# Kernel tuning notes

Hardware: AMD Instinct MI355X
Metric: run time of the kernel (lower is better)

## Reference

```python
import jax, jax.numpy as jnp
import numpy as np

SCALAR_DIM = 452          # 2 + 6 + (110+1)*4
GRID_C, GRID_H, GRID_W = 2, 32, 18
GRID_FLAT = GRID_C * GRID_H * GRID_W  # 1152
OBS_DIM = SCALAR_DIM + GRID_FLAT      # 1604
CNN_OUT, SC_OUT, HID, N_ACT = 128, 64, 128, 2305
CNN_FLAT = 64 * 8 * 5                 # 32x18 -> 16x9 -> 8x5
T, B = 256, 128


def setup_inputs() -> dict:
    key = jax.random.key(0)
    ks = jax.random.split(key, 24)
    p = lambda k, shape: jax.random.normal(k, shape, jnp.float32) * 0.02
    return dict(
        obs_seq=jax.random.uniform(ks[0], (T, B, OBS_DIM), jnp.float32),
        h0=jnp.zeros((1, B, HID), jnp.float32),
        c0=jnp.zeros((1, B, HID), jnp.float32),
        done_mask=jax.random.randint(ks[1], (T, B), 0, 2) > 0,
        conv1_w=p(ks[2], (32, GRID_C, 3, 3)), conv1_b=jnp.zeros((32,), jnp.float32),
        conv2_w=p(ks[3], (64, 32, 3, 3)),     conv2_b=jnp.zeros((64,), jnp.float32),
        conv3_w=p(ks[4], (64, 64, 3, 3)),     conv3_b=jnp.zeros((64,), jnp.float32),
        fc_w=p(ks[5], (CNN_OUT, CNN_FLAT)),   fc_b=jnp.zeros((CNN_OUT,), jnp.float32),
        s1_w=p(ks[6], (64, SCALAR_DIM)),      s1_b=jnp.zeros((64,), jnp.float32),
        s2_w=p(ks[7], (SC_OUT, 64)),          s2_b=jnp.zeros((SC_OUT,), jnp.float32),
        w_ih=p(ks[8], (4 * HID, CNN_OUT + SC_OUT)),
        w_hh=p(ks[9], (4 * HID, HID)),
        b_ih=jnp.zeros((4 * HID,), jnp.float32),
        b_hh=jnp.zeros((4 * HID,), jnp.float32),
        pol_w=p(ks[10], (N_ACT, HID)), pol_b=jnp.zeros((N_ACT,), jnp.float32),
        val_w=p(ks[11], (1, HID)),     val_b=jnp.zeros((1,), jnp.float32),
    )


def _conv(x, w, b, stride):
    y = jax.lax.conv_general_dilated(
        x, w, (stride, stride), ((1, 1), (1, 1)),
        dimension_numbers=("NCHW", "OIHW", "NCHW"))
    return y + b[None, :, None, None]


def reference(obs_seq, h0, c0, done_mask,
              conv1_w, conv1_b, conv2_w, conv2_b, conv3_w, conv3_b,
              fc_w, fc_b, s1_w, s1_b, s2_w, s2_b,
              w_ih, w_hh, b_ih, b_hh, pol_w, pol_b, val_w, val_b):
    Tt, Bb, _ = obs_seq.shape
    flat = obs_seq.reshape(Tt * Bb, -1)
    scalars = flat[:, :SCALAR_DIM]
    grid = flat[:, SCALAR_DIM:SCALAR_DIM + GRID_FLAT].reshape(-1, GRID_C, GRID_H, GRID_W)

    # CNN encoder
    x = jax.nn.relu(_conv(grid, conv1_w, conv1_b, 1))
    x = jax.nn.relu(_conv(x, conv2_w, conv2_b, 2))
    x = jax.nn.relu(_conv(x, conv3_w, conv3_b, 2))
    cnn = jax.nn.relu(x.reshape(x.shape[0], -1) @ fc_w.T + fc_b)

    # scalar MLP
    sc = jax.nn.relu(jax.nn.relu(scalars @ s1_w.T + s1_b) @ s2_w.T + s2_b)

    emb = jnp.concatenate([cnn, sc], axis=-1).reshape(Tt, Bb, -1)  # (T,B,192)

    # episode-reset mask applied BEFORE each step (for t>0, from done[t-1])
    keep = jnp.concatenate(
        [jnp.ones((1, Bb), jnp.float32),
         1.0 - done_mask[:-1].astype(jnp.float32)], axis=0)[..., None]  # (T,B,1)

    def step(carry, inp):
        h, c = carry
        x_t, k_t = inp
        h = h * k_t
        c = c * k_t
        g = x_t @ w_ih.T + h @ w_hh.T + b_ih + b_hh
        i, f, gg, o = jnp.split(g, 4, axis=-1)  # torch gate order i,f,g,o
        c = jax.nn.sigmoid(f) * c + jax.nn.sigmoid(i) * jnp.tanh(gg)
        h = jax.nn.sigmoid(o) * jnp.tanh(c)
        return (h, c), h

    (h_f, c_f), outs = jax.lax.scan(step, (h0[0], c0[0]), (emb, keep))

    logits = outs @ pol_w.T + pol_b   # (T,B,n_actions)
    values = outs @ val_w.T + val_b   # (T,B,1)
    return logits, values, h_f[None], c_f[None]
```

## Files before the change

kernel.cpp:

```cpp
#include <hip/hip_runtime.h>


typedef __attribute__((ext_vector_type(8))) short v8s;
typedef __attribute__((ext_vector_type(4))) float v4f;
typedef __attribute__((ext_vector_type(4))) unsigned int v4u;

#define DEV static __device__ __forceinline__

DEV unsigned int cvtpk(float lo, float hi){
  unsigned int d;
  asm("v_cvt_pk_bf16_f32 %0, %1, %2" : "=v"(d) : "v"(lo), "v"(hi));
  return d;
}
DEV unsigned short f2bf(float x){ return (unsigned short)(cvtpk(x, x) & 0xffffu); }
DEV float bf2f(unsigned short h){ return __uint_as_float(((unsigned int)h) << 16); }
DEV unsigned int pkbf(float a, float b){ return cvtpk(a, b); }
DEV v4f MFMA(v8s a, v8s b, v4f c){ return __builtin_amdgcn_mfma_f32_16x16x32_bf16(a, b, c, 0, 0, 0); }
DEV v4f vzero(){ v4f z = {0.f, 0.f, 0.f, 0.f}; return z; }
DEV float relu(float x){ return x > 0.f ? x : 0.f; }
DEV float sigm(float x){ return 1.0f / (1.0f + __expf(-x)); }
DEV float tanhfast(float x){
  x = fminf(15.0f, fmaxf(-15.0f, x));
  float e = __expf(2.0f * x);
  return (e - 1.0f) / (e + 1.0f);
}
DEV uint2 pack4(v4f a, float4 b){
  return make_uint2(cvtpk(relu(a[0]+b.x), relu(a[1]+b.y)),
                    cvtpk(relu(a[2]+b.z), relu(a[3]+b.w)));
}
union U8S { v4u u4; v8s s8; };

__global__ __launch_bounds__(256) void pack_all(
    const float* __restrict__ c1w, const float* __restrict__ c2w,
    const float* __restrict__ c3w, const float* __restrict__ fcw,
    const float* __restrict__ s1w, const float* __restrict__ s2w,
    const float* __restrict__ wih, const float* __restrict__ whh,
    const float* __restrict__ pw,
    unsigned short* __restrict__ w1p, unsigned short* __restrict__ w2p,
    unsigned short* __restrict__ w3p, unsigned short* __restrict__ fcp,
    unsigned short* __restrict__ s1p, unsigned short* __restrict__ s2p,
    unsigned short* __restrict__ lsp, unsigned short* __restrict__ pop){
  int b = blockIdx.x;
  const float *src, *src2 = nullptr; unsigned short* dst;
  int N, K, KS, CI, mode, rel;
  if      (b < 4)   { src=c1w; dst=w1p; N=32;  K=24;  KS=1;  CI=2;  mode=4; rel=b; }
  else if (b < 76)  { src=c2w; dst=w2p; N=64;  K=288; KS=9;  CI=32; mode=1; rel=b-4; }
  else if (b < 220) { src=c3w; dst=w3p; N=64;  K=576; KS=18; CI=64; mode=1; rel=b-76; }
  else if (b < 1500){ src=fcw; dst=fcp; N=128; K=2560;KS=80; CI=0;  mode=2; rel=b-220; }
  else if (b < 1620){ src=s1w; dst=s1p; N=64;  K=452; KS=15; CI=0;  mode=0; rel=b-1500; }
  else if (b < 1636){ src=s2w; dst=s2p; N=64;  K=64;  KS=2;  CI=0;  mode=0; rel=b-1620; }
  else if (b < 2276){ src=wih; src2=whh; dst=lsp; N=512; K=320; KS=10; CI=0; mode=3; rel=b-1636; }
  else              { src=pw;  dst=pop; N=2305;K=128; KS=4;  CI=0;  mode=0; rel=b-2276; }
  int idx = rel * 256 + threadIdx.x;
  int e  = idx & 7;
  int l  = (idx >> 3) & 63;
  int fs = idx >> 9;
  int ks = fs % KS;
  int nt = fs / KS;
  int n = nt * 16 + (l & 15);
  int k = ks * 32 + (l >> 4) * 8 + e;
  float v = 0.f;
  if (n < N && k < K){
    if (mode == 0)      v = src[n * K + k];
    else if (mode == 1){ int p9 = k / CI, ci = k - p9 * CI; v = src[(n * CI + ci) * 9 + p9]; }
    else if (mode == 2){ int pos = k >> 6, ci = k & 63;     v = src[n * 2560 + ci * 40 + pos]; }
    else if (mode == 3) v = (k < 192) ? src[n * 192 + k] : src2[n * 128 + (k - 192)];
    else { int dy = k >> 3, r = k & 7, dx = r >> 1, ci = r & 1;
           if (dx < 3) v = src[(n * 2 + ci) * 9 + dy * 3 + dx]; }
  }
  dst[idx] = f2bf(v);
}

__global__ __launch_bounds__(512) void bias_kernel(const float* __restrict__ bih,
    const float* __restrict__ bhh, float* __restrict__ bias512){
  int t = threadIdx.x;
  if (t < 512) bias512[t] = bih[t] + bhh[t];
}

__global__ __launch_bounds__(256) void mlp_kernel(const float* __restrict__ obs,
    const unsigned short* __restrict__ s1p, const unsigned short* __restrict__ s2p,
    const float* __restrict__ s1b, const float* __restrict__ s2b,
    unsigned short* __restrict__ emb){
  __shared__ __align__(16) unsigned short xl[32 * 488];
  __shared__ __align__(16) unsigned short h1[32 * 72];
  int tid = threadIdx.x, w = tid >> 6, l = tid & 63, i = l & 15, u = l >> 4;
  long s0 = (long)blockIdx.x * 32;
  for (int idx = tid; idx < 32 * 113; idx += 256){
    int r = idx / 113, q = idx - r * 113;
    float4 v = *(const float4*)&obs[(s0 + r) * 1604 + q * 4];
    *(uint2*)&xl[r * 488 + q * 4] = make_uint2(pkbf(v.x, v.y), pkbf(v.z, v.w));
  }
  for (int idx = tid; idx < 32 * 28; idx += 256){
    int r = idx / 28, k = 452 + (idx - r * 28);
    xl[r * 488 + k] = 0;
  }
  __syncthreads();
  v4f acc0 = vzero(), acc1 = vzero();
  const v8s* F1 = (const v8s*)s1p;
  #pragma unroll
  for (int ks = 0; ks < 15; ++ks){
    v8s bb = F1[(w * 15 + ks) * 64 + l];
    v8s aa0 = *(const v8s*)&xl[(0 * 16 + i) * 488 + ks * 32 + u * 8];
    v8s aa1 = *(const v8s*)&xl[(1 * 16 + i) * 488 + ks * 32 + u * 8];
    acc0 = MFMA(aa0, bb, acc0);
    acc1 = MFMA(aa1, bb, acc1);
  }
  float b1 = s1b[w * 16 + i];
  #pragma unroll
  for (int r = 0; r < 4; ++r){
    float v0 = relu(acc0[r] + b1);
    float v1 = relu(acc1[r] + b1);
    h1[(u * 4 + r) * 72 + w * 16 + i] = f2bf(v0);
    h1[(16 + u * 4 + r) * 72 + w * 16 + i] = f2bf(v1);
  }
  __syncthreads();
  v4f a20 = vzero(), a21 = vzero();
  const v8s* F2 = (const v8s*)s2p;
  #pragma unroll
  for (int ks = 0; ks < 2; ++ks){
    v8s bb = F2[(w * 2 + ks) * 64 + l];
    v8s aa0 = *(const v8s*)&h1[(0 * 16 + i) * 72 + ks * 32 + u * 8];
    v8s aa1 = *(const v8s*)&h1[(1 * 16 + i) * 72 + ks * 32 + u * 8];
    a20 = MFMA(aa0, bb, a20);
    a21 = MFMA(aa1, bb, a21);
  }
  float b2 = s2b[w * 16 + i];
  #pragma unroll
  for (int r = 0; r < 4; ++r){
    float v0 = relu(a20[r] + b2);
    float v1 = relu(a21[r] + b2);
    emb[(s0 + u * 4 + r) * 192 + 128 + w * 16 + i] = f2bf(v0);
    emb[(s0 + 16 + u * 4 + r) * 192 + 128 + w * 16 + i] = f2bf(v1);
  }
}

#define ACT1o 0
#define ACT2o 43520
#define GRIDo 68864
#define SWZ(p) ((((p) >> 1) & 7) << 4)

__global__ __launch_bounds__(256, 2) void conv_kernel(const float* __restrict__ obs,
    const unsigned short* __restrict__ w1p, const unsigned short* __restrict__ w2p,
    const unsigned short* __restrict__ w3p,
    const float* __restrict__ b1v, const float* __restrict__ b2v, const float* __restrict__ b3v,
    unsigned short* __restrict__ act3g){
  __shared__ __align__(16) char lds[74496];
  int tid = threadIdx.x, w = tid >> 6, l = tid & 63, i = l & 15, u = l >> 4;
  int nh = w & 1, mh = w >> 1;
  const v8s* W1 = (const v8s*)w1p;
  const v8s* W2 = (const v8s*)w2p;
  const v8s* W3 = (const v8s*)w3p;
  v8s w1f0 = W1[l], w1f1 = W1[64 + l];
  float4 bc1a = *(const float4*)&b1v[u * 4];
  float4 bc1b = *(const float4*)&b1v[16 + u * 4];
  float4 bc2a = *(const float4*)&b2v[nh * 32 + u * 4];
  float4 bc2b = *(const float4*)&b2v[nh * 32 + 16 + u * 4];
  float4 bc3a = *(const float4*)&b3v[nh * 32 + u * 4];
  float4 bc3b = *(const float4*)&b3v[nh * 32 + 16 + u * 4];
  for (int idx = tid; idx < 18624; idx += 256) *(unsigned int*)(lds + idx * 4) = 0u;
  int soff[4];
  #pragma unroll
  for (int j = 0; j < 4; ++j){
    int p = tid * 4 + j, r = p / 18, c = p - r * 18;
    soff[j] = ((r + 1) * 20 + (c + 1)) * 4;
  }
  __syncthreads();
  long sbase = (long)blockIdx.x * 64;
  if (tid < 144){
    const float4* gp = (const float4*)(obs + sbase * 1604 + 452);
    float4 a = gp[tid], b = gp[tid + 144];
    *(unsigned int*)(lds + GRIDo + soff[0]) = pkbf(a.x, b.x);
    *(unsigned int*)(lds + GRIDo + soff[1]) = pkbf(a.y, b.y);
    *(unsigned int*)(lds + GRIDo + soff[2]) = pkbf(a.z, b.z);
    *(unsigned int*)(lds + GRIDo + soff[3]) = pkbf(a.w, b.w);
  }
  __syncthreads();

  int pos3_0 = (mh ? 1 : 0) * 16 + i;
  int pos3_1r = 32 + i;
  int pos3_1 = pos3_1r > 39 ? 39 : pos3_1r;
  int oh30 = pos3_0 / 5, ow30 = pos3_0 - oh30 * 5;
  int oh31 = pos3_1 / 5, ow31 = pos3_1 - oh31 * 5;
  int pr3_0 = (2 * oh30) * 11 + 2 * ow30;
  int pr3_1 = (2 * oh31) * 11 + 2 * ow31;

  for (int it = 0; it < 64; ++it){
    long s = sbase + it;
    int gbo = GRIDo + (it & 1) * 2816;
    int z2; asm("s_mov_b32 %0, 0" : "=s"(z2) : "s"(it));
    v8s w2f[2][9];
    #pragma unroll
    for (int jj = 0; jj < 2; ++jj)
      #pragma unroll
      for (int t = 0; t < 9; ++t) w2f[jj][t] = W2[((nh * 2 + jj) * 9 + t) * 64 + l + z2];
    float4 pa, pb; bool pf = (it < 63) && (tid < 144);
    if (pf){
      const float4* gp = (const float4*)(obs + (s + 1) * 1604 + 452);
      pa = gp[tid]; pb = gp[tid + 144];
    }
    #pragma unroll
    for (int k = 0; k < 9; ++k){
      int ntl = w + 4 * k;
      int pos = ntl * 16 + i;
      int oh = pos / 18, ow = pos - oh * 18;
      int glin = gbo + ((oh + u) * 20 + ow) * 4;
      U8S gv;
      gv.u4.x = *(const unsigned int*)(lds + glin);
      gv.u4.y = *(const unsigned int*)(lds + glin + 4);
      gv.u4.z = *(const unsigned int*)(lds + glin + 8);
      gv.u4.w = *(const unsigned int*)(lds + glin + 12);
      v4f a0 = MFMA(w1f0, gv.s8, vzero());
      v4f a1 = MFMA(w1f1, gv.s8, vzero());
      int p1 = (oh + 1) * 20 + (ow + 1);
      int sA = SWZ(p1);
      *(uint2*)(lds + ACT1o + ((p1 * 64 + u * 8) ^ sA))      = pack4(a0, bc1a);
      *(uint2*)(lds + ACT1o + ((p1 * 64 + 32 + u * 8) ^ sA)) = pack4(a1, bc1b);
    }
    __syncthreads();
    for (int ntl = mh; ntl < 9; ntl += 2){
      int pos2 = ntl * 16 + i;
      int oh = pos2 / 9, ow = pos2 - oh * 9;
      int pr0 = (2 * oh) * 20 + 2 * ow;
      v4f a0 = vzero(), a1 = vzero();
      #pragma unroll
      for (int dy = 0; dy < 3; ++dy)
        #pragma unroll
        for (int dx = 0; dx < 3; ++dx){
          int p = pr0 + dy * 20 + dx;
          int byte = (p * 64 + u * 16) ^ SWZ(p);
          v8s bf = *(const v8s*)(lds + ACT1o + byte);
          a0 = MFMA(w2f[0][dy * 3 + dx], bf, a0);
          a1 = MFMA(w2f[1][dy * 3 + dx], bf, a1);
        }
      int p2 = (oh + 1) * 11 + (ow + 1);
      int sB = SWZ(p2);
      *(uint2*)(lds + ACT2o + ((p2 * 128 + nh * 64 + u * 8) ^ sB))      = pack4(a0, bc2a);
      *(uint2*)(lds + ACT2o + ((p2 * 128 + nh * 64 + 32 + u * 8) ^ sB)) = pack4(a1, bc2b);
    }
    if (pf){
      int gbn = GRIDo + ((it + 1) & 1) * 2816;
      *(unsigned int*)(lds + gbn + soff[0]) = pkbf(pa.x, pb.x);
      *(unsigned int*)(lds + gbn + soff[1]) = pkbf(pa.y, pb.y);
      *(unsigned int*)(lds + gbn + soff[2]) = pkbf(pa.z, pb.z);
      *(unsigned int*)(lds + gbn + soff[3]) = pkbf(pa.w, pb.w);
    }
    __syncthreads();
    {
      int z3; asm("s_mov_b32 %0, 0" : "=s"(z3) : "s"(it));
      v4f c300 = vzero(), c301 = vzero(), c310 = vzero(), c311 = vzero();
      #pragma unroll
      for (int ksh = 0; ksh < 2; ++ksh){
        const int t0 = ksh * 5, tc = ksh ? 4 : 5;
        v8s w3q[2][5][2];
        #pragma unroll
        for (int j = 0; j < 2; ++j)
          #pragma unroll
          for (int tt = 0; tt < 5; ++tt){
            if (tt < tc){
              #pragma unroll
              for (int h = 0; h < 2; ++h)
                w3q[j][tt][h] = W3[((2 * nh + j) * 18 + 2 * (t0 + tt) + h) * 64 + l + z3];
            }
          }
        #pragma unroll
        for (int tt = 0; tt < 5; ++tt){
          if (tt < tc){
            int tap = t0 + tt, dy = tap / 3, dx = tap - dy * 3;
            int dpp = dy * 11 + dx;
            #pragma unroll
            for (int h = 0; h < 2; ++h){
              {
                int p = pr3_0 + dpp;
                int byte = (p * 128 + h * 64 + u * 16) ^ SWZ(p);
                v8s bf = *(const v8s*)(lds + ACT2o + byte);
                c300 = MFMA(w3q[0][tt][h], bf, c300);
                c301 = MFMA(w3q[1][tt][h], bf, c301);
              }
              if (mh == 0){
                int p = pr3_1 + dpp;
                int byte = (p * 128 + h * 64 + u * 16) ^ SWZ(p);
                v8s bf = *(const v8s*)(lds + ACT2o + byte);
                c310 = MFMA(w3q[0][tt][h], bf, c310);
                c311 = MFMA(w3q[1][tt][h], bf, c311);
              }
            }
          }
        }
      }
      unsigned short* dg = act3g + s * 2560;
      *(uint2*)(dg + pos3_0 * 64 + nh * 32 + u * 4)      = pack4(c300, bc3a);
      *(uint2*)(dg + pos3_0 * 64 + nh * 32 + 16 + u * 4) = pack4(c301, bc3b);
      if (mh == 0 && pos3_1r < 40){
        *(uint2*)(dg + pos3_1r * 64 + nh * 32 + u * 4)      = pack4(c310, bc3a);
        *(uint2*)(dg + pos3_1r * 64 + nh * 32 + 16 + u * 4) = pack4(c311, bc3b);
      }
    }
  }
}

__global__ __launch_bounds__(256) void fc_kernel(const unsigned short* __restrict__ act3g,
    const unsigned short* __restrict__ fcp, const float* __restrict__ fcb,
    unsigned short* __restrict__ emb){
  __shared__ __align__(16) unsigned short al[64 * 264];
  int tid = threadIdx.x, w = tid >> 6, l = tid & 63, i = l & 15, u = l >> 4;
  long s0 = (long)blockIdx.x * 64;
  v4f acc[4][2];
  #pragma unroll
  for (int mt = 0; mt < 4; ++mt){ acc[mt][0] = vzero(); acc[mt][1] = vzero(); }
  const v8s* F = (const v8s*)fcp;
  for (int kc = 0; kc < 10; ++kc){
    __syncthreads();
    for (int idx = tid; idx < 64 * 32; idx += 256){
      int r = idx >> 5, q = idx & 31;
      *(v8s*)&al[r * 264 + q * 8] = *(const v8s*)&act3g[(s0 + r) * 2560 + kc * 256 + q * 8];
    }
    __syncthreads();
    #pragma unroll
    for (int ksl = 0; ksl < 8; ++ksl){
      v8s b0 = F[((w * 2 + 0) * 80 + kc * 8 + ksl) * 64 + l];
      v8s b1 = F[((w * 2 + 1) * 80 + kc * 8 + ksl) * 64 + l];
      #pragma unroll
      for (int mt = 0; mt < 4; ++mt){
        v8s aa = *(const v8s*)&al[(mt * 16 + i) * 264 + ksl * 32 + u * 8];
        acc[mt][0] = MFMA(aa, b0, acc[mt][0]);
        acc[mt][1] = MFMA(aa, b1, acc[mt][1]);
      }
    }
  }
  float fb0 = fcb[(w * 2) * 16 + i], fb1 = fcb[(w * 2 + 1) * 16 + i];
  #pragma unroll
  for (int mt = 0; mt < 4; ++mt)
    #pragma unroll
    for (int r = 0; r < 4; ++r){
      float v0 = relu(acc[mt][0][r] + fb0);
      float v1 = relu(acc[mt][1][r] + fb1);
      emb[(s0 + mt * 16 + u * 4 + r) * 192 + (w * 2) * 16 + i] = f2bf(v0);
      emb[(s0 + mt * 16 + u * 4 + r) * 192 + (w * 2 + 1) * 16 + i] = f2bf(v1);
    }
}

__global__ __launch_bounds__(256) void segprep_kernel(const void* __restrict__ dmask,
    unsigned int* __restrict__ segs, int4* __restrict__ gtab, int* __restrict__ meta){
  __shared__ int cnt[257], off[257], place[257];
  __shared__ int notInt;
  int tid = threadIdx.x;
  for (int idx = tid; idx < 257; idx += 256){ cnt[idx] = 0; place[idx] = 0; }
  if (tid == 0) notInt = 0;
  __syncthreads();
  const unsigned char* p8 = (const unsigned char*)dmask;
  int nz = 0;
  for (int idx = tid; idx < 2048; idx += 256)
    if (p8[idx * 4 + 1] | p8[idx * 4 + 2] | p8[idx * 4 + 3]) nz = 1;
  if (nz) notInt = 1;
  __syncthreads();
  bool m32 = (notInt == 0);
  const int* p32 = (const int*)dmask;
  if (tid < 128){
    int b = tid, ts = 0;
    for (int t = 0; t < 256; ++t){
      bool d = (t == 255) ? true : (m32 ? (p32[t * 128 + b] != 0) : (p8[t * 128 + b] != 0));
      if (d){ atomicAdd(&cnt[t - ts + 1], 1); ts = t + 1; }
    }
  }
  __syncthreads();
  if (tid == 0){
    int acc = 0;
    for (int len = 1; len <= 256; ++len){ off[len] = acc; acc += cnt[len]; }
    int G = 0;
    for (int len = 1; len <= 256; ++len){
      int c = cnt[len], g = 0;
      while (c > 0){
        int take = c < 32 ? c : 32;
        gtab[G] = make_int4(len, off[len] + g * 32, take, 0);
        ++G; c -= 32; ++g;
      }
    }
    meta[0] = G;
  }
  __syncthreads();
  if (tid < 128){
    int b = tid, ts = 0;
    for (int t = 0; t < 256; ++t){
      bool d = (t == 255) ? true : (m32 ? (p32[t * 128 + b] != 0) : (p8[t * 128 + b] != 0));
      if (d){
        int len = t - ts + 1;
        int slot = off[len] + atomicAdd(&place[len], 1);
        segs[slot] = (unsigned int)(b | (ts << 8));
        ts = t + 1;
      }
    }
  }
}

__global__ __launch_bounds__(512) void lstm_kernel(
    const unsigned short* __restrict__ emb, const unsigned short* __restrict__ lstmp,
    const float* __restrict__ bias512,
    const float* __restrict__ h0, const float* __restrict__ c0,
    const unsigned int* __restrict__ segs, const int4* __restrict__ gtab,
    const int* __restrict__ meta,
    unsigned short* __restrict__ outsb, float* __restrict__ hf, float* __restrict__ cf){
  int grp = blockIdx.x;
  if (grp >= meta[0]) return;
  int4 gd = gtab[grp];
  int len = gd.x, base = gd.y, nseg = gd.z;
  __shared__ __align__(16) unsigned short hbuf[2][32 * 136];
  __shared__ int sb[32], st[32];
  int tid = threadIdx.x, w = tid >> 6, l = tid & 63, i = l & 15, u = l >> 4;
  if (tid < 32){
    unsigned int sv = segs[base + (tid < nseg ? tid : 0)];
    sb[tid] = (int)(sv & 127u);
    st[tid] = (int)((sv >> 8) & 255u);
  }
  __syncthreads();
  int j = w * 16 + i;
  float cst[2][4];
  #pragma unroll
  for (int mt = 0; mt < 2; ++mt)
    #pragma unroll
    for (int r = 0; r < 4; ++r){
      int slot = mt * 16 + u * 4 + r;
      float cv = 0.f, hv = 0.f;
      if (st[slot] == 0){ cv = c0[sb[slot] * 128 + j]; hv = h0[sb[slot] * 128 + j]; }
      cst[mt][r] = cv;
      hbuf[0][slot * 136 + j] = f2bf(hv);
    }
  float bi = bias512[j], bff = bias512[128 + j], bg = bias512[256 + j], bo = bias512[384 + j];
  int bA0 = sb[i], tA0 = st[i];
  int bA1 = sb[16 + i], tA1 = st[16 + i];
  __syncthreads();
  const v8s* LP = (const v8s*)lstmp;
  for (int step = 0; step < len; ++step){
    int pb = step & 1;
    v4f gi0 = vzero(), gi1 = vzero(), gf0 = vzero(), gf1 = vzero();
    v4f gg0 = vzero(), gg1 = vzero(), go0 = vzero(), go1 = vzero();
    #pragma unroll
    for (int ks = 0; ks < 10; ++ks){
      v8s a0, a1;
      if (ks < 6){
        a0 = *(const v8s*)&emb[((long)(tA0 + step) * 128 + bA0) * 192 + ks * 32 + u * 8];
        a1 = *(const v8s*)&emb[((long)(tA1 + step) * 128 + bA1) * 192 + ks * 32 + u * 8];
      } else {
        int koff = (ks - 6) * 32 + u * 8;
        a0 = *(const v8s*)&hbuf[pb][i * 136 + koff];
        a1 = *(const v8s*)&hbuf[pb][(16 + i) * 136 + koff];
      }
      v8s b_i = LP[((w) * 10 + ks) * 64 + l];
      v8s b_f = LP[((w + 8) * 10 + ks) * 64 + l];
      v8s b_g = LP[((w + 16) * 10 + ks) * 64 + l];
      v8s b_o = LP[((w + 24) * 10 + ks) * 64 + l];
      gi0 = MFMA(a0, b_i, gi0); gi1 = MFMA(a1, b_i, gi1);
      gf0 = MFMA(a0, b_f, gf0); gf1 = MFMA(a1, b_f, gf1);
      gg0 = MFMA(a0, b_g, gg0); gg1 = MFMA(a1, b_g, gg1);
      go0 = MFMA(a0, b_o, go0); go1 = MFMA(a1, b_o, go1);
    }
    #pragma unroll
    for (int mt = 0; mt < 2; ++mt)
      #pragma unroll
      for (int r = 0; r < 4; ++r){
        int slot = mt * 16 + u * 4 + r;
        float giv = mt ? gi1[r] : gi0[r];
        float gfv = mt ? gf1[r] : gf0[r];
        float ggv = mt ? gg1[r] : gg0[r];
        float gov = mt ? go1[r] : go0[r];
        float iv = sigm(giv + bi);
        float fv = sigm(gfv + bff);
        float gv = tanhfast(ggv + bg);
        float ov = sigm(gov + bo);
        float cv = fv * cst[mt][r] + iv * gv;
        cst[mt][r] = cv;
        float hv = ov * tanhfast(cv);
        unsigned short hb = f2bf(hv);
        hbuf[pb ^ 1][slot * 136 + j] = hb;
        if (slot < nseg){
          outsb[((long)(st[slot] + step) * 128 + sb[slot]) * 128 + j] = hb;
          if (st[slot] + len == 256 && step == len - 1){
            hf[sb[slot] * 128 + j] = hv;
            cf[sb[slot] * 128 + j] = cv;
          }
        }
      }
    __syncthreads();
  }
}

__global__ __launch_bounds__(256) void heads_kernel(const unsigned short* __restrict__ outsb,
    const unsigned short* __restrict__ polp, const float* __restrict__ polb,
    const float* __restrict__ vw, const float* __restrict__ vb,
    float* __restrict__ logits, float* __restrict__ values){
  __shared__ __align__(16) unsigned short al[64 * 136];
  int tid = threadIdx.x, w = tid >> 6, l = tid & 63, i = l & 15, u = l >> 4;
  long s0 = (long)blockIdx.x * 64;
  for (int idx = tid; idx < 64 * 16; idx += 256){
    int r = idx >> 4, q = idx & 15;
    *(v8s*)&al[r * 136 + q * 8] = *(const v8s*)&outsb[(s0 + r) * 128 + q * 8];
  }
  __syncthreads();
  v8s af[4][4];
  #pragma unroll
  for (int mt = 0; mt < 4; ++mt)
    #pragma unroll
    for (int ks = 0; ks < 4; ++ks)
      af[mt][ks] = *(const v8s*)&al[(mt * 16 + i) * 136 + ks * 32 + u * 8];
  const v8s* P = (const v8s*)polp;
  for (int nt = w; nt < 145; nt += 4){
    v4f acc[4];
    #pragma unroll
    for (int mt = 0; mt < 4; ++mt) acc[mt] = vzero();
    #pragma unroll
    for (int ks = 0; ks < 4; ++ks){
      v8s bb = P[(nt * 4 + ks) * 64 + l];
      #pragma unroll
      for (int mt = 0; mt < 4; ++mt) acc[mt] = MFMA(af[mt][ks], bb, acc[mt]);
    }
    int n = nt * 16 + i;
    if (n < 2305){
      float pbv = polb[n];
      #pragma unroll
      for (int mt = 0; mt < 4; ++mt)
        #pragma unroll
        for (int r = 0; r < 4; ++r)
          logits[(s0 + mt * 16 + u * 4 + r) * 2305 + n] = acc[mt][r] + pbv;
    }
  }
  float vacc = 0.f;
  #pragma unroll
  for (int g = 0; g < 4; ++g){
    float4 vA = *(const float4*)&vw[g * 32 + u * 8];
    float4 vB = *(const float4*)&vw[g * 32 + u * 8 + 4];
    v8s xv = *(const v8s*)&al[(w * 16 + i) * 136 + g * 32 + u * 8];
    vacc += bf2f((unsigned short)xv[0]) * vA.x + bf2f((unsigned short)xv[1]) * vA.y
          + bf2f((unsigned short)xv[2]) * vA.z + bf2f((unsigned short)xv[3]) * vA.w
          + bf2f((unsigned short)xv[4]) * vB.x + bf2f((unsigned short)xv[5]) * vB.y
          + bf2f((unsigned short)xv[6]) * vB.z + bf2f((unsigned short)xv[7]) * vB.w;
  }
  vacc += __shfl_xor(vacc, 16);
  vacc += __shfl_xor(vacc, 32);
  if (u == 0) values[s0 + w * 16 + i] = vacc + vb[0];
}

extern "C" void kernel_launch(void* const* d_in, const int* in_sizes, int n_in,
                              void* d_out, int out_size, void* d_ws, size_t ws_size,
                              hipStream_t stream){
  (void)in_sizes; (void)n_in; (void)out_size; (void)ws_size;
  const float* obs = (const float*)d_in[0];
  const float* h0  = (const float*)d_in[1];
  const float* c0  = (const float*)d_in[2];
  const void*  dm  = d_in[3];
  const float* c1w = (const float*)d_in[4];  const float* c1b = (const float*)d_in[5];
  const float* c2w = (const float*)d_in[6];  const float* c2b = (const float*)d_in[7];
  const float* c3w = (const float*)d_in[8];  const float* c3b = (const float*)d_in[9];
  const float* fcw = (const float*)d_in[10]; const float* fcb = (const float*)d_in[11];
  const float* s1w = (const float*)d_in[12]; const float* s1b = (const float*)d_in[13];
  const float* s2w = (const float*)d_in[14]; const float* s2b = (const float*)d_in[15];
  const float* wih = (const float*)d_in[16]; const float* whh = (const float*)d_in[17];
  const float* bih = (const float*)d_in[18]; const float* bhh = (const float*)d_in[19];
  const float* pw  = (const float*)d_in[20]; const float* pb  = (const float*)d_in[21];
  const float* vw  = (const float*)d_in[22]; const float* vb  = (const float*)d_in[23];

  char* ws = (char*)d_ws;
  size_t off = 0;
  auto take = [&](size_t sz)->char*{
    char* p = ws + off; off = (off + sz + 255) & ~(size_t)255; return p;
  };
  unsigned short* emb    = (unsigned short*)take(32768UL * 192 * 2);
  unsigned short* outsb  = (unsigned short*)take(32768UL * 128 * 2);
  unsigned short* w1p    = (unsigned short*)take(1024UL * 2);
  unsigned short* w2p    = (unsigned short*)take(18432UL * 2);
  unsigned short* w3p    = (unsigned short*)take(36864UL * 2);
  unsigned short* fcp    = (unsigned short*)take(327680UL * 2);
  unsigned short* s1p    = (unsigned short*)take(30720UL * 2);
  unsigned short* s2p    = (unsigned short*)take(4096UL * 2);
  unsigned short* lsp    = (unsigned short*)take(163840UL * 2);
  unsigned short* pop    = (unsigned short*)take(296960UL * 2);
  float*          b512   = (float*)take(512UL * 4);
  unsigned int*   segs   = (unsigned int*)take(32768UL * 4);
  int4*           gtab   = (int4*)take(1280UL * 16);
  int*            meta   = (int*)take(256);

  float* outp   = (float*)d_out;
  float* logits = outp;
  float* values = outp + 75530240L;
  float* hf     = outp + 75563008L;
  float* cf     = outp + 75579392L;
  unsigned short* act3g = (unsigned short*)d_out;

  dim3 b256(256), b512t(512);
  pack_all<<<dim3(3436), b256, 0, stream>>>(c1w, c2w, c3w, fcw, s1w, s2w, wih, whh, pw,
                                            w1p, w2p, w3p, fcp, s1p, s2p, lsp, pop);
  bias_kernel<<<dim3(1), b512t, 0, stream>>>(bih, bhh, b512);
  segprep_kernel<<<dim3(1), b256, 0, stream>>>(dm, segs, gtab, meta);
  mlp_kernel<<<dim3(1024), b256, 0, stream>>>(obs, s1p, s2p, s1b, s2b, emb);
  conv_kernel<<<dim3(512), b256, 0, stream>>>(obs, w1p, w2p, w3p, c1b, c2b, c3b, act3g);
  fc_kernel<<<dim3(512), b256, 0, stream>>>(act3g, fcp, fcb, emb);
  lstm_kernel<<<dim3(1280), b512t, 0, stream>>>(emb, lsp, b512, h0, c0, segs, gtab, meta,
                                                outsb, hf, cf);
  heads_kernel<<<dim3(512), b256, 0, stream>>>(outsb, pop, pb, vw, vb, logits, values);
}
```

Baseline: 1.025 ms.

## Merge small prep kernels and fuse MLP with FC; hoist conv weights and offsets

Bias summation and segment preparation become extra blocks of the weight-packing kernel, and the scalar MLP is merged with the CNN FC into a single embed kernel, cutting the launch count from eight to five. In the conv kernel, conv2 weight fragments and per-iteration LDS address offsets are hoisted out of the 64-iteration loop. Biases are now preloaded as the MFMA accumulator initial values instead of being added at pack time. Hoisting raises register pressure in a kernel launched with two blocks per CU, which risks spills.

```diff
diff --git a/kernel.cpp b/kernel.cpp
--- a/kernel.cpp
+++ b/kernel.cpp
@@ -28,6 +28,11 @@
   return make_uint2(cvtpk(relu(a[0]+b.x), relu(a[1]+b.y)),
                     cvtpk(relu(a[2]+b.z), relu(a[3]+b.w)));
 }
+DEV uint2 pack4r(v4f a){
+  return make_uint2(cvtpk(relu(a[0]), relu(a[1])),
+                    cvtpk(relu(a[2]), relu(a[3])));
+}
+DEV v4f b2v4(float4 b){ v4f a; a[0]=b.x; a[1]=b.y; a[2]=b.z; a[3]=b.w; return a; }
 union U8S { v4u u4; v8s s8; };
 
 __global__ __launch_bounds__(256) void pack_all(
@@ -39,8 +44,68 @@
     unsigned short* __restrict__ w1p, unsigned short* __restrict__ w2p,
     unsigned short* __restrict__ w3p, unsigned short* __restrict__ fcp,
     unsigned short* __restrict__ s1p, unsigned short* __restrict__ s2p,
-    unsigned short* __restrict__ lsp, unsigned short* __restrict__ pop){
+    unsigned short* __restrict__ lsp, unsigned short* __restrict__ pop,
+    const void* __restrict__ dmask, const float* __restrict__ bih,
+    const float* __restrict__ bhh, float* __restrict__ bias512,
+    unsigned int* __restrict__ segs, int4* __restrict__ gtab, int* __restrict__ meta){
+  __shared__ int sp[772];
   int b = blockIdx.x;
+  int tid = threadIdx.x;
+  if (b == 3437){
+    bias512[tid] = bih[tid] + bhh[tid];
+    bias512[tid + 256] = bih[tid + 256] + bhh[tid + 256];
+    return;
+  }
+  if (b == 3436){
+    int* cnt = sp; int* off = sp + 257; int* place = sp + 514;
+    for (int idx = tid; idx < 257; idx += 256){ cnt[idx] = 0; place[idx] = 0; }
+    if (tid == 0) sp[771] = 0;
+    __syncthreads();
+    const unsigned char* p8 = (const unsigned char*)dmask;
+    int nz = 0;
+    for (int idx = tid; idx < 2048; idx += 256)
+      if (p8[idx * 4 + 1] | p8[idx * 4 + 2] | p8[idx * 4 + 3]) nz = 1;
+    if (nz) sp[771] = 1;
+    __syncthreads();
+    bool m32 = (sp[771] == 0);
+    const int* p32 = (const int*)dmask;
+    if (tid < 128){
+      int bb = tid, ts = 0;
+      for (int t = 0; t < 256; ++t){
+        bool d = (t == 255) ? true : (m32 ? (p32[t * 128 + bb] != 0) : (p8[t * 128 + bb] != 0));
+        if (d){ atomicAdd(&cnt[t - ts + 1], 1); ts = t + 1; }
+      }
+    }
+    __syncthreads();
+    if (tid == 0){
+      int acc = 0;
+      for (int len = 1; len <= 256; ++len){ off[len] = acc; acc += cnt[len]; }
+      int G = 0;
+      for (int len = 1; len <= 256; ++len){
+        int c = cnt[len], g = 0;
+        while (c > 0){
+          int take = c < 32 ? c : 32;
+          gtab[G] = make_int4(len, off[len] + g * 32, take, 0);
+          ++G; c -= 32; ++g;
+        }
+      }
+      meta[0] = G;
+    }
+    __syncthreads();
+    if (tid < 128){
+      int bb = tid, ts = 0;
+      for (int t = 0; t < 256; ++t){
+        bool d = (t == 255) ? true : (m32 ? (p32[t * 128 + bb] != 0) : (p8[t * 128 + bb] != 0));
+        if (d){
+          int len = t - ts + 1;
+          int slot = off[len] + atomicAdd(&place[len], 1);
+          segs[slot] = (unsigned int)(bb | (ts << 8));
+          ts = t + 1;
+        }
+      }
+    }
+    return;
+  }
   const float *src, *src2 = nullptr; unsigned short* dst;
   int N, K, KS, CI, mode, rel;
   if      (b < 4)   { src=c1w; dst=w1p; N=32;  K=24;  KS=1;  CI=2;  mode=4; rel=b; }
@@ -51,7 +116,7 @@
   else if (b < 1636){ src=s2w; dst=s2p; N=64;  K=64;  KS=2;  CI=0;  mode=0; rel=b-1620; }
   else if (b < 2276){ src=wih; src2=whh; dst=lsp; N=512; K=320; KS=10; CI=0; mode=3; rel=b-1636; }
   else              { src=pw;  dst=pop; N=2305;K=128; KS=4;  CI=0;  mode=0; rel=b-2276; }
-  int idx = rel * 256 + threadIdx.x;
+  int idx = rel * 256 + tid;
   int e  = idx & 7;
   int l  = (idx >> 3) & 63;
   int fs = idx >> 9;
@@ -71,69 +136,6 @@
   dst[idx] = f2bf(v);
 }
 
-__global__ __launch_bounds__(512) void bias_kernel(const float* __restrict__ bih,
-    const float* __restrict__ bhh, float* __restrict__ bias512){
-  int t = threadIdx.x;
-  if (t < 512) bias512[t] = bih[t] + bhh[t];
-}
-
-__global__ __launch_bounds__(256) void mlp_kernel(const float* __restrict__ obs,
-    const unsigned short* __restrict__ s1p, const unsigned short* __restrict__ s2p,
-    const float* __restrict__ s1b, const float* __restrict__ s2b,
-    unsigned short* __restrict__ emb){
-  __shared__ __align__(16) unsigned short xl[32 * 488];
-  __shared__ __align__(16) unsigned short h1[32 * 72];
-  int tid = threadIdx.x, w = tid >> 6, l = tid & 63, i = l & 15, u = l >> 4;
-  long s0 = (long)blockIdx.x * 32;
-  for (int idx = tid; idx < 32 * 113; idx += 256){
-    int r = idx / 113, q = idx - r * 113;
-    float4 v = *(const float4*)&obs[(s0 + r) * 1604 + q * 4];
-    *(uint2*)&xl[r * 488 + q * 4] = make_uint2(pkbf(v.x, v.y), pkbf(v.z, v.w));
-  }
-  for (int idx = tid; idx < 32 * 28; idx += 256){
-    int r = idx / 28, k = 452 + (idx - r * 28);
-    xl[r * 488 + k] = 0;
-  }
-  __syncthreads();
-  v4f acc0 = vzero(), acc1 = vzero();
-  const v8s* F1 = (const v8s*)s1p;
-  #pragma unroll
-  for (int ks = 0; ks < 15; ++ks){
-    v8s bb = F1[(w * 15 + ks) * 64 + l];
-    v8s aa0 = *(const v8s*)&xl[(0 * 16 + i) * 488 + ks * 32 + u * 8];
-    v8s aa1 = *(const v8s*)&xl[(1 * 16 + i) * 488 + ks * 32 + u * 8];
-    acc0 = MFMA(aa0, bb, acc0);
-    acc1 = MFMA(aa1, bb, acc1);
-  }
-  float b1 = s1b[w * 16 + i];
-  #pragma unroll
-  for (int r = 0; r < 4; ++r){
-    float v0 = relu(acc0[r] + b1);
-    float v1 = relu(acc1[r] + b1);
-    h1[(u * 4 + r) * 72 + w * 16 + i] = f2bf(v0);
-    h1[(16 + u * 4 + r) * 72 + w * 16 + i] = f2bf(v1);
-  }
-  __syncthreads();
-  v4f a20 = vzero(), a21 = vzero();
-  const v8s* F2 = (const v8s*)s2p;
-  #pragma unroll
-  for (int ks = 0; ks < 2; ++ks){
-    v8s bb = F2[(w * 2 + ks) * 64 + l];
-    v8s aa0 = *(const v8s*)&h1[(0 * 16 + i) * 72 + ks * 32 + u * 8];
-    v8s aa1 = *(const v8s*)&h1[(1 * 16 + i) * 72 + ks * 32 + u * 8];
-    a20 = MFMA(aa0, bb, a20);
-    a21 = MFMA(aa1, bb, a21);
-  }
-  float b2 = s2b[w * 16 + i];
-  #pragma unroll
-  for (int r = 0; r < 4; ++r){
-    float v0 = relu(a20[r] + b2);
-    float v1 = relu(a21[r] + b2);
-    emb[(s0 + u * 4 + r) * 192 + 128 + w * 16 + i] = f2bf(v0);
-    emb[(s0 + 16 + u * 4 + r) * 192 + 128 + w * 16 + i] = f2bf(v1);
-  }
-}
-
 #define ACT1o 0
 #define ACT2o 43520
 #define GRIDo 68864
@@ -151,12 +153,17 @@
   const v8s* W2 = (const v8s*)w2p;
   const v8s* W3 = (const v8s*)w3p;
   v8s w1f0 = W1[l], w1f1 = W1[64 + l];
-  float4 bc1a = *(const float4*)&b1v[u * 4];
-  float4 bc1b = *(const float4*)&b1v[16 + u * 4];
-  float4 bc2a = *(const float4*)&b2v[nh * 32 + u * 4];
-  float4 bc2b = *(const float4*)&b2v[nh * 32 + 16 + u * 4];
-  float4 bc3a = *(const float4*)&b3v[nh * 32 + u * 4];
-  float4 bc3b = *(const float4*)&b3v[nh * 32 + 16 + u * 4];
+  v8s w2f[2][9];
+  #pragma unroll
+  for (int jj = 0; jj < 2; ++jj)
+    #pragma unroll
+    for (int t = 0; t < 9; ++t) w2f[jj][t] = W2[((nh * 2 + jj) * 9 + t) * 64 + l];
+  v4f bv1a = b2v4(*(const float4*)&b1v[u * 4]);
+  v4f bv1b = b2v4(*(const float4*)&b1v[16 + u * 4]);
+  v4f bv2a = b2v4(*(const float4*)&b2v[nh * 32 + u * 4]);
+  v4f bv2b = b2v4(*(const float4*)&b2v[nh * 32 + 16 + u * 4]);
+  v4f bv3a = b2v4(*(const float4*)&b3v[nh * 32 + u * 4]);
+  v4f bv3b = b2v4(*(const float4*)&b3v[nh * 32 + 16 + u * 4]);
   for (int idx = tid; idx < 18624; idx += 256) *(unsigned int*)(lds + idx * 4) = 0u;
   int soff[4];
   #pragma unroll
@@ -176,6 +183,38 @@
   }
   __syncthreads();
 
+  int goffk[9], wAk[9], wBk[9];
+  #pragma unroll
+  for (int k = 0; k < 9; ++k){
+    int ntl = w + 4 * k;
+    int pos = ntl * 16 + i;
+    int oh = pos / 18, ow = pos - oh * 18;
+    goffk[k] = ((oh + u) * 20 + ow) * 4;
+    int p1 = (oh + 1) * 20 + (ow + 1);
+    wAk[k] = ACT1o + ((p1 * 64 + u * 8) ^ SWZ(p1));
+    wBk[k] = ACT1o + ((p1 * 64 + 32 + u * 8) ^ SWZ(p1));
+  }
+  int pr2k[5], w2Ak[5], w2Bk[5];
+  #pragma unroll
+  for (int kk = 0; kk < 5; ++kk){
+    int ntl = mh + 2 * kk;
+    int ntc = ntl < 9 ? ntl : 0;
+    int pos2 = ntc * 16 + i;
+    int oh = pos2 / 9, ow = pos2 - oh * 9;
+    pr2k[kk] = (2 * oh) * 20 + 2 * ow;
+    int p2 = (oh + 1) * 11 + (ow + 1);
+    w2Ak[kk] = ACT2o + ((p2 * 128 + nh * 64 + u * 8) ^ SWZ(p2));
+    w2Bk[kk] = w2Ak[kk] ^ 32;
+  }
+  #pragma unroll
+  for (int kk = 0; kk < 5; ++kk){
+    int ntl = mh + 2 * kk;
+    int ntc = ntl < 9 ? ntl : 0;
+    int pos2 = ntc * 16 + i;
+    int oh = pos2 / 9, ow = pos2 - oh * 9;
+    int p2 = (oh + 1) * 11 + (ow + 1);
+    w2Bk[kk] = ACT2o + ((p2 * 128 + nh * 64 + 32 + u * 8) ^ SWZ(p2));
+  }
   int pos3_0 = (mh ? 1 : 0) * 16 + i;
   int pos3_1r = 32 + i;
   int pos3_1 = pos3_1r > 39 ? 39 : pos3_1r;
@@ -187,12 +226,6 @@
   for (int it = 0; it < 64; ++it){
     long s = sbase + it;
     int gbo = GRIDo + (it & 1) * 2816;
-    int z2; asm("s_mov_b32 %0, 0" : "=s"(z2) : "s"(it));
-    v8s w2f[2][9];
-    #pragma unroll
-    for (int jj = 0; jj < 2; ++jj)
-      #pragma unroll
-      for (int t = 0; t < 9; ++t) w2f[jj][t] = W2[((nh * 2 + jj) * 9 + t) * 64 + l + z2];
     float4 pa, pb; bool pf = (it < 63) && (tid < 144);
     if (pf){
       const float4* gp = (const float4*)(obs + (s + 1) * 1604 + 452);
@@ -200,42 +233,35 @@
     }
     #pragma unroll
     for (int k = 0; k < 9; ++k){
-      int ntl = w + 4 * k;
-      int pos = ntl * 16 + i;
-      int oh = pos / 18, ow = pos - oh * 18;
-      int glin = gbo + ((oh + u) * 20 + ow) * 4;
+      int glin = gbo + goffk[k];
       U8S gv;
       gv.u4.x = *(const unsigned int*)(lds + glin);
       gv.u4.y = *(const unsigned int*)(lds + glin + 4);
       gv.u4.z = *(const unsigned int*)(lds + glin + 8);
       gv.u4.w = *(const unsigned int*)(lds + glin + 12);
-      v4f a0 = MFMA(w1f0, gv.s8, vzero());
-      v4f a1 = MFMA(w1f1, gv.s8, vzero());
-      int p1 = (oh + 1) * 20 + (ow + 1);
-      int sA = SWZ(p1);
-      *(uint2*)(lds + ACT1o + ((p1 * 64 + u * 8) ^ sA))      = pack4(a0, bc1a);
-      *(uint2*)(lds + ACT1o + ((p1 * 64 + 32 + u * 8) ^ sA)) = pack4(a1, bc1b);
-    }
-    __syncthreads();
-    for (int ntl = mh; ntl < 9; ntl += 2){
-      int pos2 = ntl * 16 + i;
-      int oh = pos2 / 9, ow = pos2 - oh * 9;
-      int pr0 = (2 * oh) * 20 + 2 * ow;
-      v4f a0 = vzero(), a1 = vzero();
-      #pragma unroll
-      for (int dy = 0; dy < 3; ++dy)
+      v4f a0 = MFMA(w1f0, gv.s8, bv1a);
+      v4f a1 = MFMA(w1f1, gv.s8, bv1b);
+      *(uint2*)(lds + wAk[k]) = pack4r(a0);
+      *(uint2*)(lds + wBk[k]) = pack4r(a1);
+    }
+    __syncthreads();
+    #pragma unroll
+    for (int kk = 0; kk < 5; ++kk){
+      if (mh + 2 * kk < 9){
+        v4f a0 = bv2a, a1 = bv2b;
         #pragma unroll
-        for (int dx = 0; dx < 3; ++dx){
-          int p = pr0 + dy * 20 + dx;
-          int byte = (p * 64 + u * 16) ^ SWZ(p);
-          v8s bf = *(const v8s*)(lds + ACT1o + byte);
-          a0 = MFMA(w2f[0][dy * 3 + dx], bf, a0);
-          a1 = MFMA(w2f[1][dy * 3 + dx], bf, a1);
-        }
-      int p2 = (oh + 1) * 11 + (ow + 1);
-      int sB = SWZ(p2);
-      *(uint2*)(lds + ACT2o + ((p2 * 128 + nh * 64 + u * 8) ^ sB))      = pack4(a0, bc2a);
-      *(uint2*)(lds + ACT2o + ((p2 * 128 + nh * 64 + 32 + u * 8) ^ sB)) = pack4(a1, bc2b);
+        for (int dy = 0; dy < 3; ++dy)
+          #pragma unroll
+          for (int dx = 0; dx < 3; ++dx){
+            int p = pr2k[kk] + dy * 20 + dx;
+            int byte = (p * 64 + u * 16) ^ SWZ(p);
+            v8s bf = *(const v8s*)(lds + ACT1o + byte);
+            a0 = MFMA(w2f[0][dy * 3 + dx], bf, a0);
+            a1 = MFMA(w2f[1][dy * 3 + dx], bf, a1);
+          }
+        *(uint2*)(lds + w2Ak[kk]) = pack4r(a0);
+        *(uint2*)(lds + w2Bk[kk]) = pack4r(a1);
+      }
     }
     if (pf){
       int gbn = GRIDo + ((it + 1) & 1) * 2816;
@@ -247,7 +273,7 @@
     __syncthreads();
     {
       int z3; asm("s_mov_b32 %0, 0" : "=s"(z3) : "s"(it));
-      v4f c300 = vzero(), c301 = vzero(), c310 = vzero(), c311 = vzero();
+      v4f c300 = bv3a, c301 = bv3b, c310 = bv3a, c311 = bv3b;
       #pragma unroll
       for (int ksh = 0; ksh < 2; ++ksh){
         const int t0 = ksh * 5, tc = ksh ? 4 : 5;
@@ -288,106 +314,112 @@
         }
       }
       unsigned short* dg = act3g + s * 2560;
-      *(uint2*)(dg + pos3_0 * 64 + nh * 32 + u * 4)      = pack4(c300, bc3a);
-      *(uint2*)(dg + pos3_0 * 64 + nh * 32 + 16 + u * 4) = pack4(c301, bc3b);
+      *(uint2*)(dg + pos3_0 * 64 + nh * 32 + u * 4)      = pack4r(c300);
+      *(uint2*)(dg + pos3_0 * 64 + nh * 32 + 16 + u * 4) = pack4r(c301);
       if (mh == 0 && pos3_1r < 40){
-        *(uint2*)(dg + pos3_1r * 64 + nh * 32 + u * 4)      = pack4(c310, bc3a);
-        *(uint2*)(dg + pos3_1r * 64 + nh * 32 + 16 + u * 4) = pack4(c311, bc3b);
-      }
-    }
-  }
-}
-
-__global__ __launch_bounds__(256) void fc_kernel(const unsigned short* __restrict__ act3g,
-    const unsigned short* __restrict__ fcp, const float* __restrict__ fcb,
+        *(uint2*)(dg + pos3_1r * 64 + nh * 32 + u * 4)      = pack4r(c310);
+        *(uint2*)(dg + pos3_1r * 64 + nh * 32 + 16 + u * 4) = pack4r(c311);
+      }
+    }
+  }
+}
+
+__global__ __launch_bounds__(256) void embed_kernel(
+    const unsigned short* __restrict__ act3g, const unsigned short* __restrict__ fcp,
+    const float* __restrict__ fcb,
+    const float* __restrict__ obs, const unsigned short* __restrict__ s1p,
+    const unsigned short* __restrict__ s2p,
+    const float* __restrict__ s1b, const float* __restrict__ s2b,
     unsigned short* __restrict__ emb){
-  __shared__ __align__(16) unsigned short al[64 * 264];
+  __shared__ __align__(16) unsigned short shb[17920];
+  int bid = blockIdx.x;
   int tid = threadIdx.x, w = tid >> 6, l = tid & 63, i = l & 15, u = l >> 4;
-  long s0 = (long)blockIdx.x * 64;
-  v4f acc[4][2];
-  #pragma unroll
-  for (int mt = 0; mt < 4; ++mt){ acc[mt][0] = vzero(); acc[mt][1] = vzero(); }
-  const v8s* F = (const v8s*)fcp;
-  for (int kc = 0; kc < 10; ++kc){
-    __syncthreads();
-    for (int idx = tid; idx < 64 * 32; idx += 256){
-      int r = idx >> 5, q = idx & 31;
-      *(v8s*)&al[r * 264 + q * 8] = *(const v8s*)&act3g[(s0 + r) * 2560 + kc * 256 + q * 8];
-    }
-    __syncthreads();
-    #pragma unroll
-    for (int ksl = 0; ksl < 8; ++ksl){
-      v8s b0 = F[((w * 2 + 0) * 80 + kc * 8 + ksl) * 64 + l];
-      v8s b1 = F[((w * 2 + 1) * 80 + kc * 8 + ksl) * 64 + l];
+  if (bid < 512){
+    unsigned short* al = shb;
+    long s0 = (long)bid * 64;
+    v4f acc[4][2];
+    #pragma unroll
+    for (int mt = 0; mt < 4; ++mt){ acc[mt][0] = vzero(); acc[mt][1] = vzero(); }
+    const v8s* F = (const v8s*)fcp;
+    for (int kc = 0; kc < 10; ++kc){
+      __syncthreads();
+      for (int idx = tid; idx < 64 * 32; idx += 256){
+        int r = idx >> 5, q = idx & 31;
+        *(v8s*)&al[r * 264 + q * 8] = *(const v8s*)&act3g[(s0 + r) * 2560 + kc * 256 + q * 8];
+      }
+      __syncthreads();
       #pragma unroll
-      for (int mt = 0; mt < 4; ++mt){
-        v8s aa = *(const v8s*)&al[(mt * 16 + i) * 264 + ksl * 32 + u * 8];
-        acc[mt][0] = MFMA(aa, b0, acc[mt][0]);
-        acc[mt][1] = MFMA(aa, b1, acc[mt][1]);
-      }
-    }
-  }
-  float fb0 = fcb[(w * 2) * 16 + i], fb1 = fcb[(w * 2 + 1) * 16 + i];
-  #pragma unroll
-  for (int mt = 0; mt < 4; ++mt)
+      for (int ksl = 0; ksl < 8; ++ksl){
+        v8s b0 = F[((w * 2 + 0) * 80 + kc * 8 + ksl) * 64 + l];
+        v8s b1 = F[((w * 2 + 1) * 80 + kc * 8 + ksl) * 64 + l];
+        #pragma unroll
+        for (int mt = 0; mt < 4; ++mt){
+          v8s aa = *(const v8s*)&al[(mt * 16 + i) * 264 + ksl * 32 + u * 8];
+          acc[mt][0] = MFMA(aa, b0, acc[mt][0]);
+          acc[mt][1] = MFMA(aa, b1, acc[mt][1]);
+        }
+      }
+    }
+    float fb0 = fcb[(w * 2) * 16 + i], fb1 = fcb[(w * 2 + 1) * 16 + i];
+    #pragma unroll
+    for (int mt = 0; mt < 4; ++mt)
+      #pragma unroll
+      for (int r = 0; r < 4; ++r){
+        float v0 = relu(acc[mt][0][r] + fb0);
+        float v1 = relu(acc[mt][1][r] + fb1);
+        emb[(s0 + mt * 16 + u * 4 + r) * 192 + (w * 2) * 16 + i] = f2bf(v0);
+        emb[(s0 + mt * 16 + u * 4 + r) * 192 + (w * 2 + 1) * 16 + i] = f2bf(v1);
+      }
+  } else {
+    unsigned short* xl = shb;
+    unsigned short* h1 = shb + 15616;
+    long s0 = (long)(bid - 512) * 32;
+    for (int idx = tid; idx < 32 * 113; idx += 256){
+      int r = idx / 113, q = idx - r * 113;
+      float4 v = *(const float4*)&obs[(s0 + r) * 1604 + q * 4];
+      *(uint2*)&xl[r * 488 + q * 4] = make_uint2(pkbf(v.x, v.y), pkbf(v.z, v.w));
+    }
+    for (int idx = tid; idx < 32 * 28; idx += 256){
+      int r = idx / 28, k = 452 + (idx - r * 28);
+      xl[r * 488 + k] = 0;
+    }
+    __syncthreads();
+    v4f acc0 = vzero(), acc1 = vzero();
+    const v8s* F1 = (const v8s*)s1p;
+    #pragma unroll
+    for (int ks = 0; ks < 15; ++ks){
+      v8s bb = F1[(w * 15 + ks) * 64 + l];
+      v8s aa0 = *(const v8s*)&xl[(0 * 16 + i) * 488 + ks * 32 + u * 8];
+      v8s aa1 = *(const v8s*)&xl[(1 * 16 + i) * 488 + ks * 32 + u * 8];
+      acc0 = MFMA(aa0, bb, acc0);
+      acc1 = MFMA(aa1, bb, acc1);
+    }
+    float b1 = s1b[w * 16 + i];
     #pragma unroll
     for (int r = 0; r < 4; ++r){
-      float v0 = relu(acc[mt][0][r] + fb0);
-      float v1 = relu(acc[mt][1][r] + fb1);
-      emb[(s0 + mt * 16 + u * 4 + r) * 192 + (w * 2) * 16 + i] = f2bf(v0);
-      emb[(s0 + mt * 16 + u * 4 + r) * 192 + (w * 2 + 1) * 16 + i] = f2bf(v1);
-    }
-}
-
-__global__ __launch_bounds__(256) void segprep_kernel(const void* __restrict__ dmask,
-    unsigned int* __restrict__ segs, int4* __restrict__ gtab, int* __restrict__ meta){
-  __shared__ int cnt[257], off[257], place[257];
-  __shared__ int notInt;
-  int tid = threadIdx.x;
-  for (int idx = tid; idx < 257; idx += 256){ cnt[idx] = 0; place[idx] = 0; }
-  if (tid == 0) notInt = 0;
-  __syncthreads();
-  const unsigned char* p8 = (const unsigned char*)dmask;
-  int nz = 0;
-  for (int idx = tid; idx < 2048; idx += 256)
-    if (p8[idx * 4 + 1] | p8[idx * 4 + 2] | p8[idx * 4 + 3]) nz = 1;
-  if (nz) notInt = 1;
-  __syncthreads();
-  bool m32 = (notInt == 0);
-  const int* p32 = (const int*)dmask;
-  if (tid < 128){
-    int b = tid, ts = 0;
-    for (int t = 0; t < 256; ++t){
-      bool d = (t == 255) ? true : (m32 ? (p32[t * 128 + b] != 0) : (p8[t * 128 + b] != 0));
-      if (d){ atomicAdd(&cnt[t - ts + 1], 1); ts = t + 1; }
-    }
-  }
-  __syncthreads();
-  if (tid == 0){
-    int acc = 0;
-    for (int len = 1; len <= 256; ++len){ off[len] = acc; acc += cnt[len]; }
-    int G = 0;
-    for (int len = 1; len <= 256; ++len){
-      int c = cnt[len], g = 0;
-      while (c > 0){
-        int take = c < 32 ? c : 32;
-        gtab[G] = make_int4(len, off[len] + g * 32, take, 0);
-        ++G; c -= 32; ++g;
-      }
-    }
-    meta[0] = G;
-  }
-  __syncthreads();
-  if (tid < 128){
-    int b = tid, ts = 0;
-    for (int t = 0; t < 256; ++t){
-      bool d = (t == 255) ? true : (m32 ? (p32[t * 128 + b] != 0) : (p8[t * 128 + b] != 0));
-      if (d){
-        int len = t - ts + 1;
-        int slot = off[len] + atomicAdd(&place[len], 1);
-        segs[slot] = (unsigned int)(b | (ts << 8));
-        ts = t + 1;
-      }
+      float v0 = relu(acc0[r] + b1);
+      float v1 = relu(acc1[r] + b1);
+      h1[(u * 4 + r) * 72 + w * 16 + i] = f2bf(v0);
+      h1[(16 + u * 4 + r) * 72 + w * 16 + i] = f2bf(v1);
+    }
+    __syncthreads();
+    v4f a20 = vzero(), a21 = vzero();
+    const v8s* F2 = (const v8s*)s2p;
+    #pragma unroll
+    for (int ks = 0; ks < 2; ++ks){
+      v8s bb = F2[(w * 2 + ks) * 64 + l];
+      v8s aa0 = *(const v8s*)&h1[(0 * 16 + i) * 72 + ks * 32 + u * 8];
+      v8s aa1 = *(const v8s*)&h1[(1 * 16 + i) * 72 + ks * 32 + u * 8];
+      a20 = MFMA(aa0, bb, a20);
+      a21 = MFMA(aa1, bb, a21);
+    }
+    float b2 = s2b[w * 16 + i];
+    #pragma unroll
+    for (int r = 0; r < 4; ++r){
+      float v0 = relu(a20[r] + b2);
+      float v1 = relu(a21[r] + b2);
+      emb[(s0 + u * 4 + r) * 192 + 128 + w * 16 + i] = f2bf(v0);
+      emb[(s0 + 16 + u * 4 + r) * 192 + 128 + w * 16 + i] = f2bf(v1);
     }
   }
 }
@@ -585,13 +617,11 @@
   unsigned short* act3g = (unsigned short*)d_out;
 
   dim3 b256(256), b512t(512);
-  pack_all<<<dim3(3436), b256, 0, stream>>>(c1w, c2w, c3w, fcw, s1w, s2w, wih, whh, pw,
-                                            w1p, w2p, w3p, fcp, s1p, s2p, lsp, pop);
-  bias_kernel<<<dim3(1), b512t, 0, stream>>>(bih, bhh, b512);
-  segprep_kernel<<<dim3(1), b256, 0, stream>>>(dm, segs, gtab, meta);
-  mlp_kernel<<<dim3(1024), b256, 0, stream>>>(obs, s1p, s2p, s1b, s2b, emb);
+  pack_all<<<dim3(3438), b256, 0, stream>>>(c1w, c2w, c3w, fcw, s1w, s2w, wih, whh, pw,
+                                            w1p, w2p, w3p, fcp, s1p, s2p, lsp, pop,
+                                            dm, bih, bhh, b512, segs, gtab, meta);
   conv_kernel<<<dim3(512), b256, 0, stream>>>(obs, w1p, w2p, w3p, c1b, c2b, c3b, act3g);
-  fc_kernel<<<dim3(512), b256, 0, stream>>>(act3g, fcp, fcb, emb);
+  embed_kernel<<<dim3(1536), b256, 0, stream>>>(act3g, fcp, fcb, obs, s1p, s2p, s1b, s2b, emb);
   lstm_kernel<<<dim3(1280), b512t, 0, stream>>>(emb, lsp, b512, h0, c0, segs, gtab, meta,
                                                 outsb, hf, cf);
   heads_kernel<<<dim3(512), b256, 0, stream>>>(outsb, pop, pb, vw, vb, logits, values);
```

Result: slower. 2.158 ms (+110.6%).
